# Optimization experiments

Measured on AMD Instinct MI355X. Metric: run time of the kernel, lower is better.

## Reference

```python
import jax, jax.numpy as jnp
import numpy as np

N, E, H, NIN, DD = 10000, 160000, 128, 128, 256
SCALE = 30.0
EPS = 1e-5

def _ln(x, g, b):
    mu = jnp.mean(x, axis=-1, keepdims=True)
    var = jnp.mean((x - mu) ** 2, axis=-1, keepdims=True)
    return (x - mu) * jax.lax.rsqrt(var + EPS) * g + b

def _gelu(x):
    return jax.nn.gelu(x, approximate=False)  # torch nn.GELU default (erf)

def setup_inputs() -> dict:
    key = jax.random.key(0)
    ks = jax.random.split(key, 16)
    def w(k, i, o):
        return jax.random.normal(k, (i, o), jnp.float32) * (1.0 / np.sqrt(i))
    return {
        "h_V": jax.random.normal(ks[0], (N, H), jnp.float32),
        "h_E": jax.random.normal(ks[1], (E, H + NIN), jnp.float32),
        "edge_idx": jax.random.randint(ks[2], (2, E), 0, N, jnp.int32),
        # message MLP: (H+NIN)->H, H->H
        "m_w0": w(ks[3], H + NIN, H), "m_b0": jnp.zeros((H,), jnp.float32),
        "m_w1": w(ks[4], H, H),       "m_b1": jnp.zeros((H,), jnp.float32),
        # dense MLP: H->DD, DD->DD, final DD->H
        "d_w0": w(ks[5], H, DD),  "d_b0": jnp.zeros((DD,), jnp.float32),
        "d_w1": w(ks[6], DD, DD), "d_b1": jnp.zeros((DD,), jnp.float32),
        "d_w2": w(ks[7], DD, H),  "d_b2": jnp.zeros((H,), jnp.float32),
        # LayerNorm params
        "g1": jnp.ones((H,), jnp.float32), "be1": jnp.zeros((H,), jnp.float32),
        "g2": jnp.ones((H,), jnp.float32), "be2": jnp.zeros((H,), jnp.float32),
    }

def reference(h_V, h_E, edge_idx, m_w0, m_b0, m_w1, m_b1,
              d_w0, d_b0, d_w1, d_b1, d_w2, d_b2, g1, be1, g2, be2):
    src_idx = edge_idx[0]
    # message MLP over edges (dropout = identity at inference)
    h = _gelu(h_E @ m_w0 + m_b0)
    h_message = _gelu(h @ m_w1 + m_b1)          # [E, H]
    # scatter-sum aggregate edges -> nodes
    dh = jax.ops.segment_sum(h_message, src_idx, num_segments=N) / SCALE
    h_V = _ln(h_V + dh, g1, be1)
    # dense MLP over nodes
    d = _gelu(h_V @ d_w0 + d_b0)
    d = _gelu(d @ d_w1 + d_b1)
    dh = d @ d_w2 + d_b2
    return _ln(h_V + dh, g2, be2)
```

## Files before the change

### kernel.cpp

```cpp
#include <hip/hip_runtime.h>
#include <hip/hip_bf16.h>


typedef __attribute__((ext_vector_type(8))) short bf16x8;
typedef __attribute__((ext_vector_type(4))) float f32x4;

__device__ __forceinline__ unsigned short f2bf(float f) {
  union { float f; unsigned u; } v; v.f = f;
  return (unsigned short)((v.u + 0x7fffu + ((v.u >> 16) & 1u)) >> 16);
}
__device__ __forceinline__ unsigned pk2bf(float a, float b) {
  __hip_bfloat162 h = __float22bfloat162_rn(make_float2(a, b));
  union { __hip_bfloat162 h; unsigned u; } v; v.h = h;
  return v.u;
}
__device__ __forceinline__ unsigned short bf1(float x) {
  return (unsigned short)pk2bf(x, x);
}
__device__ __forceinline__ float bf2f(unsigned s) {
  union { unsigned u; float f; } v; v.u = s << 16;
  return v.f;
}
__device__ __forceinline__ float gelu_f(float x) {
  float x2 = x * x;
  float u2 = x * fmaf(0.0713548162f, x2, 1.5957691216f);
  float e = __expf(u2);
  float r = __builtin_amdgcn_rcpf(e + 1.0f);
  float th = fmaf(-2.0f, r, 1.0f);
  float hx = 0.5f * x;
  return fmaf(hx, th, hx);
}

__global__ void k_pack(const float* __restrict__ mw0, const float* __restrict__ mw1,
                       const float* __restrict__ dw0, const float* __restrict__ dw1,
                       const float* __restrict__ dw2,
                       unsigned short* __restrict__ pw0, unsigned short* __restrict__ pw1,
                       unsigned short* __restrict__ pd0, unsigned short* __restrict__ pd1,
                       unsigned short* __restrict__ pd2,
                       int* __restrict__ counts, int Nn) {
  int g = blockIdx.x, lane = threadIdx.x;
  int z = g * 64 + lane;
  if (z < Nn) counts[z] = 0;
  const float* src; unsigned short* dst; int K, N, WC, base;
  if (g < 64)       { src = mw0; dst = pw0; K = 256; N = 128; WC = 128; base = 0; }
  else if (g < 96)  { src = mw1; dst = pw1; K = 128; N = 128; WC = 128; base = 64; }
  else if (g < 160) { src = dw0; dst = pd0; K = 128; N = 256; WC = 64; base = 96; }
  else if (g < 288) { src = dw1; dst = pd1; K = 256; N = 256; WC = 64; base = 160; }
  else              { src = dw2; dst = pd2; K = 256; N = 128; WC = 32; base = 288; }
  int lg = g - base;
  int KS = K >> 5, CTKS = (WC >> 4) * KS;
  int w = lg / CTKS, rem = lg % CTKS, ct = rem / KS, ks = rem % KS;
  int col = w * WC + ct * 16 + (lane & 15);
  int k0 = ks * 32 + (lane >> 4) * 8;
  unsigned short o[8];
#pragma unroll
  for (int j = 0; j < 8; ++j) o[j] = f2bf(src[(size_t)(k0 + j) * N + col]);
  uint4 u;
  u.x = (unsigned)o[0] | ((unsigned)o[1] << 16);
  u.y = (unsigned)o[2] | ((unsigned)o[3] << 16);
  u.z = (unsigned)o[4] | ((unsigned)o[5] << 16);
  u.w = (unsigned)o[6] | ((unsigned)o[7] << 16);
  *(uint4*)(dst + (size_t)(lg * 64 + lane) * 8) = u;
}

__global__ void k_hist(const int* __restrict__ eidx, int* __restrict__ counts, int E) {
  int e = blockIdx.x * 256 + threadIdx.x;
  if (e < E) atomicAdd(&counts[eidx[e]], 1);
}

__global__ __launch_bounds__(1024) void k_scan(const int* __restrict__ counts,
                                               int* __restrict__ row_start,
                                               int* __restrict__ cursor, int Nn) {
  __shared__ int sm[1024];
  int t = threadIdx.x;
  int chunk = (Nn + 1023) / 1024;
  int lo = t * chunk, hi = lo + chunk;
  if (hi > Nn) hi = Nn;
  int s = 0;
  for (int i = lo; i < hi; ++i) s += counts[i];
  sm[t] = s;
  __syncthreads();
  for (int o = 1; o < 1024; o <<= 1) {
    int u = (t >= o) ? sm[t - o] : 0;
    __syncthreads();
    sm[t] += u;
    __syncthreads();
  }
  int run = sm[t] - s;
  for (int i = lo; i < hi; ++i) {
    row_start[i] = run; cursor[i] = run; run += counts[i];
  }
  if (t == 1023) row_start[Nn] = sm[1023];
}

__global__ void k_scatter(const int* __restrict__ eidx, int* __restrict__ cursor,
                          int* __restrict__ eorder, int E) {
  int e = blockIdx.x * 256 + threadIdx.x;
  if (e < E) {
    int pos = atomicAdd(&cursor[eidx[e]], 1);
    eorder[pos] = e;
  }
}

__global__ __launch_bounds__(512, 2) void k_edge(
    const float* __restrict__ hE, const unsigned short* __restrict__ pw0,
    const unsigned short* __restrict__ pw1, const float* __restrict__ b0,
    const float* __restrict__ b1, unsigned short* __restrict__ hmsg, int E) {
  __shared__ __align__(16) char lds[131072];
  const int tid = threadIdx.x;
  const int wid = tid >> 6, lane = tid & 63;
  const int l15 = lane & 15, lhi = lane >> 4;
  char* Hw = lds + 98304 + wid * 4096;

  {
    const uint4* s0 = (const uint4*)pw0;
    const uint4* s1 = (const uint4*)pw1;
    uint4* d = (uint4*)lds;
#pragma unroll
    for (int i = 0; i < 12; ++i) {
      int idx = i * 512 + tid;
      d[idx] = (idx < 4096) ? s0[idx] : s1[idx - 4096];
    }
  }
  float bb0[8], bb1[8];
#pragma unroll
  for (int ct = 0; ct < 8; ++ct) {
    bb0[ct] = b0[ct * 16 + l15];
    bb1[ct] = b1[ct * 16 + l15];
  }
  __syncthreads();

  const int TILES = (E + 15) >> 4;
  const int WSLOTS = gridDim.x * 8;
  int t = blockIdx.x * 8 + wid;
  if (t >= TILES) return;

  f32x4 av[16];
  {
    int rowA = t * 16 + l15; rowA = rowA < E ? rowA : E - 1;
    const float* ap = hE + (size_t)rowA * 256 + lhi * 8;
#pragma unroll
    for (int ks = 0; ks < 8; ++ks) {
      av[2 * ks]     = *(const f32x4*)(ap + ks * 32);
      av[2 * ks + 1] = *(const f32x4*)(ap + ks * 32 + 4);
    }
  }

  for (; t < TILES; t += WSLOTS) {
    const int tn = t + WSLOTS;
    bf16x8 af[8];
#pragma unroll
    for (int ks = 0; ks < 8; ++ks) {
      union { unsigned u[4]; bf16x8 v; } pk;
      pk.u[0] = pk2bf(av[2 * ks][0], av[2 * ks][1]);
      pk.u[1] = pk2bf(av[2 * ks][2], av[2 * ks][3]);
      pk.u[2] = pk2bf(av[2 * ks + 1][0], av[2 * ks + 1][1]);
      pk.u[3] = pk2bf(av[2 * ks + 1][2], av[2 * ks + 1][3]);
      af[ks] = pk.v;
    }
    if (tn < TILES) {
      int rowA = tn * 16 + l15; rowA = rowA < E ? rowA : E - 1;
      const float* ap = hE + (size_t)rowA * 256 + lhi * 8;
#pragma unroll
      for (int ks = 0; ks < 8; ++ks) {
        av[2 * ks]     = *(const f32x4*)(ap + ks * 32);
        av[2 * ks + 1] = *(const f32x4*)(ap + ks * 32 + 4);
      }
    }

    f32x4 acc[8];
#pragma unroll
    for (int ct = 0; ct < 8; ++ct) {
      float b = bb0[ct];
      acc[ct][0] = b; acc[ct][1] = b; acc[ct][2] = b; acc[ct][3] = b;
    }
#pragma unroll
    for (int ks = 0; ks < 8; ++ks)
#pragma unroll
      for (int ct = 0; ct < 8; ++ct) {
        bf16x8 b = *(bf16x8*)(lds + (ct * 8 + ks) * 1024 + lane * 16);
        acc[ct] = __builtin_amdgcn_mfma_f32_16x16x32_bf16(af[ks], b, acc[ct], 0, 0, 0);
      }
#pragma unroll
    for (int ct = 0; ct < 8; ++ct)
#pragma unroll
      for (int j = 0; j < 4; ++j) {
        int r = lhi * 4 + j, col = ct * 16 + l15;
        *(unsigned short*)(Hw + r * 256 + ((col * 2) ^ ((r & 7) << 4))) =
            bf1(gelu_f(acc[ct][j]));
      }

    f32x4 acc2[8];
#pragma unroll
    for (int ct = 0; ct < 8; ++ct) {
      float b = bb1[ct];
      acc2[ct][0] = b; acc2[ct][1] = b; acc2[ct][2] = b; acc2[ct][3] = b;
    }
#pragma unroll
    for (int ks = 0; ks < 4; ++ks) {
      bf16x8 a = *(bf16x8*)(Hw + l15 * 256 + ((ks * 64 + lhi * 16) ^ ((l15 & 7) << 4)));
#pragma unroll
      for (int ct = 0; ct < 8; ++ct) {
        bf16x8 b = *(bf16x8*)(lds + 65536 + (ct * 4 + ks) * 1024 + lane * 16);
        acc2[ct] = __builtin_amdgcn_mfma_f32_16x16x32_bf16(a, b, acc2[ct], 0, 0, 0);
      }
    }
    const int row0 = t * 16;
#pragma unroll
    for (int ct = 0; ct < 8; ++ct)
#pragma unroll
      for (int j = 0; j < 4; ++j) {
        int r = row0 + lhi * 4 + j;
        if (r < E) {
          int col = ct * 16 + l15;
          hmsg[(size_t)r * 128 + col] = bf1(gelu_f(acc2[ct][j]));
        }
      }
  }
}

__global__ __launch_bounds__(256) void k_aggln(
    const unsigned* __restrict__ hmsg, const float2* __restrict__ hV,
    const int* __restrict__ row_start, const int* __restrict__ eorder,
    const float* __restrict__ g1, const float* __restrict__ be1,
    float2* __restrict__ hv1f, unsigned* __restrict__ hv1b, int Nn) {
  int wid = threadIdx.x >> 6, lane = threadIdx.x & 63;
  int node = blockIdx.x * 4 + wid;
  if (node >= Nn) return;
  int s = row_start[node], e = row_start[node + 1];
  float s0 = 0.f, s1 = 0.f;
  int i = s;
  for (; i + 3 < e; i += 4) {
    int e0 = eorder[i], e1 = eorder[i + 1], e2 = eorder[i + 2], e3 = eorder[i + 3];
    unsigned v0 = hmsg[(size_t)e0 * 64 + lane];
    unsigned v1 = hmsg[(size_t)e1 * 64 + lane];
    unsigned v2 = hmsg[(size_t)e2 * 64 + lane];
    unsigned v3 = hmsg[(size_t)e3 * 64 + lane];
    s0 += bf2f(v0 & 0xffffu) + bf2f(v1 & 0xffffu) + bf2f(v2 & 0xffffu) + bf2f(v3 & 0xffffu);
    s1 += bf2f(v0 >> 16) + bf2f(v1 >> 16) + bf2f(v2 >> 16) + bf2f(v3 >> 16);
  }
  for (; i < e; ++i) {
    unsigned v = hmsg[(size_t)eorder[i] * 64 + lane];
    s0 += bf2f(v & 0xffffu);
    s1 += bf2f(v >> 16);
  }
  float2 hv = hV[(size_t)node * 64 + lane];
  float x0 = hv.x + s0 * (1.f / 30.f);
  float x1 = hv.y + s1 * (1.f / 30.f);
  float sum = x0 + x1, sq = x0 * x0 + x1 * x1;
#pragma unroll
  for (int off = 32; off > 0; off >>= 1) {
    sum += __shfl_xor(sum, off);
    sq += __shfl_xor(sq, off);
  }
  float mu = sum * (1.f / 128.f);
  float var = sq * (1.f / 128.f) - mu * mu;
  float rs = rsqrtf(var + 1e-5f);
  int c = lane * 2;
  float y0 = (x0 - mu) * rs * g1[c] + be1[c];
  float y1 = (x1 - mu) * rs * g1[c + 1] + be1[c + 1];
  hv1f[(size_t)node * 64 + lane] = make_float2(y0, y1);
  hv1b[(size_t)node * 64 + lane] = (unsigned)pk2bf(y0, y1);
}

__global__ __launch_bounds__(256, 4) void k_node(
    const unsigned short* __restrict__ xb, const unsigned short* __restrict__ pd0,
    const unsigned short* __restrict__ pd1, const unsigned short* __restrict__ pd2,
    const float* __restrict__ db0, const float* __restrict__ db1,
    const float* __restrict__ db2, const float* __restrict__ hv1f,
    const float* __restrict__ g2, const float* __restrict__ be2,
    float* __restrict__ out, int Nn) {
  __shared__ __align__(16) char lds[8192 + 16384 + 16384];
  char* A0 = lds;
  char* D0 = lds + 8192;
  char* D1 = lds + 8192 + 16384;
  float* Y = (float*)D0;
  const int tid = threadIdx.x, wid = tid >> 6, lane = tid & 63;
  const int l15 = lane & 15, lhi = lane >> 4;
  const int row0 = blockIdx.x * 32;

  {
    int idx = tid;
    int r = idx >> 3, c = idx & 7;
    uint4 v = make_uint4(0u, 0u, 0u, 0u);
    if (row0 + r < Nn) v = ((const uint4*)xb)[(size_t)(row0 + r) * 16 + c * 2];
    *(uint4*)(A0 + r * 256 + ((c * 32) ^ ((r & 7) << 4))) = v;
    uint4 v2 = make_uint4(0u, 0u, 0u, 0u);
    if (row0 + r < Nn) v2 = ((const uint4*)xb)[(size_t)(row0 + r) * 16 + c * 2 + 1];
    *(uint4*)(A0 + r * 256 + (((c * 32) + 16) ^ ((r & 7) << 4))) = v2;
  }
  __syncthreads();

  {
    f32x4 acc[2][4];
#pragma unroll
    for (int ct = 0; ct < 4; ++ct) {
      float b = db0[wid * 64 + ct * 16 + l15];
#pragma unroll
      for (int mt = 0; mt < 2; ++mt) {
        acc[mt][ct][0] = b; acc[mt][ct][1] = b; acc[mt][ct][2] = b; acc[mt][ct][3] = b;
      }
    }
#pragma unroll
    for (int ks = 0; ks < 4; ++ks) {
      bf16x8 a[2];
#pragma unroll
      for (int mt = 0; mt < 2; ++mt) {
        int row = mt * 16 + l15;
        a[mt] = *(bf16x8*)(A0 + row * 256 + ((ks * 64 + lhi * 16) ^ ((row & 7) << 4)));
      }
#pragma unroll
      for (int ct = 0; ct < 4; ++ct) {
        uint4 bv = ((const uint4*)pd0)[(size_t)(wid * 16 + ct * 4 + ks) * 64 + lane];
        bf16x8 b = *(bf16x8*)&bv;
#pragma unroll
        for (int mt = 0; mt < 2; ++mt)
          acc[mt][ct] = __builtin_amdgcn_mfma_f32_16x16x32_bf16(a[mt], b, acc[mt][ct], 0, 0, 0);
      }
    }
#pragma unroll
    for (int ct = 0; ct < 4; ++ct) {
      int col = wid * 64 + ct * 16 + l15;
#pragma unroll
      for (int mt = 0; mt < 2; ++mt)
#pragma unroll
        for (int j = 0; j < 4; ++j) {
          int r = mt * 16 + lhi * 4 + j;
          *(unsigned short*)(D0 + r * 512 + ((col * 2) ^ ((r & 7) << 4))) =
              bf1(gelu_f(acc[mt][ct][j]));
        }
    }
  }
  __syncthreads();

  {
    f32x4 acc[2][4];
#pragma unroll
    for (int ct = 0; ct < 4; ++ct) {
      float b = db1[wid * 64 + ct * 16 + l15];
#pragma unroll
      for (int mt = 0; mt < 2; ++mt) {
        acc[mt][ct][0] = b; acc[mt][ct][1] = b; acc[mt][ct][2] = b; acc[mt][ct][3] = b;
      }
    }
#pragma unroll
    for (int ks = 0; ks < 8; ++ks) {
      bf16x8 a[2];
#pragma unroll
      for (int mt = 0; mt < 2; ++mt) {
        int row = mt * 16 + l15;
        a[mt] = *(bf16x8*)(D0 + row * 512 + ((ks * 64 + lhi * 16) ^ ((row & 7) << 4)));
      }
#pragma unroll
      for (int ct = 0; ct < 4; ++ct) {
        uint4 bv = ((const uint4*)pd1)[(size_t)(wid * 32 + ct * 8 + ks) * 64 + lane];
        bf16x8 b = *(bf16x8*)&bv;
#pragma unroll
        for (int mt = 0; mt < 2; ++mt)
          acc[mt][ct] = __builtin_amdgcn_mfma_f32_16x16x32_bf16(a[mt], b, acc[mt][ct], 0, 0, 0);
      }
    }
#pragma unroll
    for (int ct = 0; ct < 4; ++ct) {
      int col = wid * 64 + ct * 16 + l15;
#pragma unroll
      for (int mt = 0; mt < 2; ++mt)
#pragma unroll
        for (int j = 0; j < 4; ++j) {
          int r = mt * 16 + lhi * 4 + j;
          *(unsigned short*)(D1 + r * 512 + ((col * 2) ^ ((r & 7) << 4))) =
              bf1(gelu_f(acc[mt][ct][j]));
        }
    }
  }
  __syncthreads();

  {
    f32x4 acc[2][2];
#pragma unroll
    for (int ct = 0; ct < 2; ++ct) {
      float b = db2[wid * 32 + ct * 16 + l15];
#pragma unroll
      for (int mt = 0; mt < 2; ++mt) {
        acc[mt][ct][0] = b; acc[mt][ct][1] = b; acc[mt][ct][2] = b; acc[mt][ct][3] = b;
      }
    }
#pragma unroll
    for (int ks = 0; ks < 8; ++ks) {
      bf16x8 a[2];
#pragma unroll
      for (int mt = 0; mt < 2; ++mt) {
        int row = mt * 16 + l15;
        a[mt] = *(bf16x8*)(D1 + row * 512 + ((ks * 64 + lhi * 16) ^ ((row & 7) << 4)));
      }
#pragma unroll
      for (int ct = 0; ct < 2; ++ct) {
        uint4 bv = ((const uint4*)pd2)[(size_t)(wid * 16 + ct * 8 + ks) * 64 + lane];
        bf16x8 b = *(bf16x8*)&bv;
#pragma unroll
        for (int mt = 0; mt < 2; ++mt)
          acc[mt][ct] = __builtin_amdgcn_mfma_f32_16x16x32_bf16(a[mt], b, acc[mt][ct], 0, 0, 0);
      }
    }
    __syncthreads();
#pragma unroll
    for (int ct = 0; ct < 2; ++ct) {
      int col = wid * 32 + ct * 16 + l15;
#pragma unroll
      for (int mt = 0; mt < 2; ++mt)
#pragma unroll
        for (int j = 0; j < 4; ++j) {
          int r = mt * 16 + lhi * 4 + j;
          int grow = row0 + r;
          float res = (grow < Nn) ? hv1f[(size_t)grow * 128 + col] : 0.f;
          Y[r * 128 + col] = acc[mt][ct][j] + res;
        }
    }
  }
  __syncthreads();

  float g2a = g2[lane * 2], g2b = g2[lane * 2 + 1];
  float ba = be2[lane * 2], bbx = be2[lane * 2 + 1];
  for (int ii = 0; ii < 8; ++ii) {
    int r = wid * 8 + ii;
    int grow = row0 + r;
    if (grow >= Nn) continue;
    float2 xy = *(float2*)&Y[r * 128 + lane * 2];
    float sum = xy.x + xy.y, sq = xy.x * xy.x + xy.y * xy.y;
#pragma unroll
    for (int off = 32; off > 0; off >>= 1) {
      sum += __shfl_xor(sum, off);
      sq += __shfl_xor(sq, off);
    }
    float mu = sum * (1.f / 128.f);
    float var = sq * (1.f / 128.f) - mu * mu;
    float rs = rsqrtf(var + 1e-5f);
    float y0 = (xy.x - mu) * rs * g2a + ba;
    float y1 = (xy.y - mu) * rs * g2b + bbx;
    *(float2*)&out[(size_t)grow * 128 + lane * 2] = make_float2(y0, y1);
  }
}

extern "C" void kernel_launch(void* const* d_in, const int* in_sizes, int n_in,
                              void* d_out, int out_size, void* d_ws, size_t ws_size,
                              hipStream_t stream) {
  const float* hV  = (const float*)d_in[0];
  const float* hE  = (const float*)d_in[1];
  const int* eidx  = (const int*)d_in[2];
  const float* mw0 = (const float*)d_in[3];
  const float* mb0 = (const float*)d_in[4];
  const float* mw1 = (const float*)d_in[5];
  const float* mb1 = (const float*)d_in[6];
  const float* dw0 = (const float*)d_in[7];
  const float* db0 = (const float*)d_in[8];
  const float* dw1 = (const float*)d_in[9];
  const float* db1 = (const float*)d_in[10];
  const float* dw2 = (const float*)d_in[11];
  const float* db2 = (const float*)d_in[12];
  const float* g1  = (const float*)d_in[13];
  const float* be1 = (const float*)d_in[14];
  const float* g2  = (const float*)d_in[15];
  const float* be2 = (const float*)d_in[16];
  const int Nn = in_sizes[0] / 128;
  const int E  = in_sizes[1] / 256;

  char* ws = (char*)d_ws;
  size_t off = 0;
  auto alloc = [&](size_t bytes) -> char* {
    off = (off + 255) & ~(size_t)255;
    char* p = ws + off;
    off += bytes;
    return p;
  };
  unsigned short* hmsg = (unsigned short*)alloc((size_t)E * 128 * 2);
  float* hv1f          = (float*)alloc((size_t)Nn * 128 * 4);
  unsigned short* hv1b = (unsigned short*)alloc((size_t)Nn * 128 * 2);
  unsigned short* pw0  = (unsigned short*)alloc(32768 * 2);
  unsigned short* pw1  = (unsigned short*)alloc(16384 * 2);
  unsigned short* pd0  = (unsigned short*)alloc(32768 * 2);
  unsigned short* pd1  = (unsigned short*)alloc(65536 * 2);
  unsigned short* pd2  = (unsigned short*)alloc(32768 * 2);
  int* counts    = (int*)alloc((size_t)Nn * 4);
  int* row_start = (int*)alloc((size_t)(Nn + 1) * 4);
  int* cursor    = (int*)alloc((size_t)Nn * 4);
  int* eorder    = (int*)alloc((size_t)E * 4);

  k_pack<<<352, 64, 0, stream>>>(mw0, mw1, dw0, dw1, dw2, pw0, pw1, pd0, pd1, pd2,
                                 counts, Nn);
  k_hist<<<(E + 255) / 256, 256, 0, stream>>>(eidx, counts, E);
  k_scan<<<1, 1024, 0, stream>>>(counts, row_start, cursor, Nn);
  k_scatter<<<(E + 255) / 256, 256, 0, stream>>>(eidx, cursor, eorder, E);
  k_edge<<<256, 512, 0, stream>>>(hE, pw0, pw1, mb0, mb1, hmsg, E);
  k_aggln<<<(Nn + 3) / 4, 256, 0, stream>>>((const unsigned*)hmsg, (const float2*)hV,
                                            row_start, eorder, g1, be1,
                                            (float2*)hv1f, (unsigned*)hv1b, Nn);
  const int nt = (Nn + 31) / 32;
  k_node<<<nt, 256, 0, stream>>>(hv1b, pd0, pd1, pd2, db0, db1, db2,
                                 hv1f, g2, be2, (float*)d_out, Nn);
}
```

Before: 135.1 us.

## Process two 16-row edge tiles per wave to reuse LDS weight fragments

The edge message MLP kernel now has each wave handle 32 edge rows per iteration instead of 16. Each weight fragment loaded from LDS feeds two MFMAs, which halves LDS traffic per matrix instruction, and the per-wave scratch buffer is doubled to hold both tiles' intermediate activations. In exchange, the cross-iteration software prefetch of the next tile's h_E rows is dropped, LDS use grows to 160KB, and register pressure rises under the existing launch bounds, with a risk of spills.

```diff
diff --git a/kernel.cpp b/kernel.cpp
--- a/kernel.cpp
+++ b/kernel.cpp
@@ -106,11 +106,11 @@
     const float* __restrict__ hE, const unsigned short* __restrict__ pw0,
     const unsigned short* __restrict__ pw1, const float* __restrict__ b0,
     const float* __restrict__ b1, unsigned short* __restrict__ hmsg, int E) {
-  __shared__ __align__(16) char lds[131072];
+  __shared__ __align__(16) char lds[163840];
   const int tid = threadIdx.x;
   const int wid = tid >> 6, lane = tid & 63;
   const int l15 = lane & 15, lhi = lane >> 4;
-  char* Hw = lds + 98304 + wid * 4096;
+  char* Hw = lds + 98304 + wid * 8192;
 
   {
     const uint4* s0 = (const uint4*)pw0;
@@ -130,91 +130,104 @@
   }
   __syncthreads();
 
-  const int TILES = (E + 15) >> 4;
+  const int TILES = (E + 31) >> 5;
   const int WSLOTS = gridDim.x * 8;
-  int t = blockIdx.x * 8 + wid;
-  if (t >= TILES) return;
-
-  f32x4 av[16];
-  {
-    int rowA = t * 16 + l15; rowA = rowA < E ? rowA : E - 1;
-    const float* ap = hE + (size_t)rowA * 256 + lhi * 8;
-#pragma unroll
-    for (int ks = 0; ks < 8; ++ks) {
-      av[2 * ks]     = *(const f32x4*)(ap + ks * 32);
-      av[2 * ks + 1] = *(const f32x4*)(ap + ks * 32 + 4);
-    }
-  }
-
-  for (; t < TILES; t += WSLOTS) {
-    const int tn = t + WSLOTS;
-    bf16x8 af[8];
-#pragma unroll
-    for (int ks = 0; ks < 8; ++ks) {
-      union { unsigned u[4]; bf16x8 v; } pk;
-      pk.u[0] = pk2bf(av[2 * ks][0], av[2 * ks][1]);
-      pk.u[1] = pk2bf(av[2 * ks][2], av[2 * ks][3]);
-      pk.u[2] = pk2bf(av[2 * ks + 1][0], av[2 * ks + 1][1]);
-      pk.u[3] = pk2bf(av[2 * ks + 1][2], av[2 * ks + 1][3]);
-      af[ks] = pk.v;
-    }
-    if (tn < TILES) {
-      int rowA = tn * 16 + l15; rowA = rowA < E ? rowA : E - 1;
-      const float* ap = hE + (size_t)rowA * 256 + lhi * 8;
+  for (int t = blockIdx.x * 8 + wid; t < TILES; t += WSLOTS) {
+    const int row0 = t * 32;
+    int r0 = row0 + l15;      r0 = r0 < E ? r0 : E - 1;
+    int r1 = row0 + 16 + l15; r1 = r1 < E ? r1 : E - 1;
+    const float* ap0 = hE + (size_t)r0 * 256 + lhi * 8;
+    const float* ap1 = hE + (size_t)r1 * 256 + lhi * 8;
+
+    bf16x8 af0[8], af1[8];
+    {
+      f32x4 av0[16], av1[16];
 #pragma unroll
       for (int ks = 0; ks < 8; ++ks) {
-        av[2 * ks]     = *(const f32x4*)(ap + ks * 32);
-        av[2 * ks + 1] = *(const f32x4*)(ap + ks * 32 + 4);
-      }
-    }
-
-    f32x4 acc[8];
+        av0[2 * ks]     = *(const f32x4*)(ap0 + ks * 32);
+        av0[2 * ks + 1] = *(const f32x4*)(ap0 + ks * 32 + 4);
+      }
+#pragma unroll
+      for (int ks = 0; ks < 8; ++ks) {
+        av1[2 * ks]     = *(const f32x4*)(ap1 + ks * 32);
+        av1[2 * ks + 1] = *(const f32x4*)(ap1 + ks * 32 + 4);
+      }
+#pragma unroll
+      for (int ks = 0; ks < 8; ++ks) {
+        union { unsigned u[4]; bf16x8 v; } p0, p1;
+        p0.u[0] = pk2bf(av0[2 * ks][0], av0[2 * ks][1]);
+        p0.u[1] = pk2bf(av0[2 * ks][2], av0[2 * ks][3]);
+        p0.u[2] = pk2bf(av0[2 * ks + 1][0], av0[2 * ks + 1][1]);
+        p0.u[3] = pk2bf(av0[2 * ks + 1][2], av0[2 * ks + 1][3]);
+        af0[ks] = p0.v;
+        p1.u[0] = pk2bf(av1[2 * ks][0], av1[2 * ks][1]);
+        p1.u[1] = pk2bf(av1[2 * ks][2], av1[2 * ks][3]);
+        p1.u[2] = pk2bf(av1[2 * ks + 1][0], av1[2 * ks + 1][1]);
+        p1.u[3] = pk2bf(av1[2 * ks + 1][2], av1[2 * ks + 1][3]);
+        af1[ks] = p1.v;
+      }
+    }
+
+    f32x4 acc0[8], acc1[8];
 #pragma unroll
     for (int ct = 0; ct < 8; ++ct) {
       float b = bb0[ct];
-      acc[ct][0] = b; acc[ct][1] = b; acc[ct][2] = b; acc[ct][3] = b;
-    }
-#pragma unroll
-    for (int ks = 0; ks < 8; ++ks)
+      acc0[ct][0] = b; acc0[ct][1] = b; acc0[ct][2] = b; acc0[ct][3] = b;
+      acc1[ct] = acc0[ct];
+    }
+#pragma unroll
+    for (int ks = 0; ks < 8; ++ks) {
+      bf16x8 bfr[8];
+#pragma unroll
+      for (int ct = 0; ct < 8; ++ct)
+        bfr[ct] = *(bf16x8*)(lds + (ct * 8 + ks) * 1024 + lane * 16);
 #pragma unroll
       for (int ct = 0; ct < 8; ++ct) {
-        bf16x8 b = *(bf16x8*)(lds + (ct * 8 + ks) * 1024 + lane * 16);
-        acc[ct] = __builtin_amdgcn_mfma_f32_16x16x32_bf16(af[ks], b, acc[ct], 0, 0, 0);
-      }
+        acc0[ct] = __builtin_amdgcn_mfma_f32_16x16x32_bf16(af0[ks], bfr[ct], acc0[ct], 0, 0, 0);
+        acc1[ct] = __builtin_amdgcn_mfma_f32_16x16x32_bf16(af1[ks], bfr[ct], acc1[ct], 0, 0, 0);
+      }
+    }
 #pragma unroll
     for (int ct = 0; ct < 8; ++ct)
 #pragma unroll
       for (int j = 0; j < 4; ++j) {
-        int r = lhi * 4 + j, col = ct * 16 + l15;
-        *(unsigned short*)(Hw + r * 256 + ((col * 2) ^ ((r & 7) << 4))) =
-            bf1(gelu_f(acc[ct][j]));
-      }
-
-    f32x4 acc2[8];
+        int rr = lhi * 4 + j, col = ct * 16 + l15;
+        int sw = (col * 2) ^ ((rr & 7) << 4);
+        *(unsigned short*)(Hw + rr * 256 + sw) = bf1(gelu_f(acc0[ct][j]));
+        *(unsigned short*)(Hw + (16 + rr) * 256 + sw) = bf1(gelu_f(acc1[ct][j]));
+      }
+
+    f32x4 acc20[8], acc21[8];
 #pragma unroll
     for (int ct = 0; ct < 8; ++ct) {
       float b = bb1[ct];
-      acc2[ct][0] = b; acc2[ct][1] = b; acc2[ct][2] = b; acc2[ct][3] = b;
+      acc20[ct][0] = b; acc20[ct][1] = b; acc20[ct][2] = b; acc20[ct][3] = b;
+      acc21[ct] = acc20[ct];
     }
 #pragma unroll
     for (int ks = 0; ks < 4; ++ks) {
-      bf16x8 a = *(bf16x8*)(Hw + l15 * 256 + ((ks * 64 + lhi * 16) ^ ((l15 & 7) << 4)));
+      int off = (ks * 64 + lhi * 16) ^ ((l15 & 7) << 4);
+      bf16x8 a0 = *(bf16x8*)(Hw + l15 * 256 + off);
+      bf16x8 a1 = *(bf16x8*)(Hw + (16 + l15) * 256 + off);
+      bf16x8 bfr[8];
+#pragma unroll
+      for (int ct = 0; ct < 8; ++ct)
+        bfr[ct] = *(bf16x8*)(lds + 65536 + (ct * 4 + ks) * 1024 + lane * 16);
 #pragma unroll
       for (int ct = 0; ct < 8; ++ct) {
-        bf16x8 b = *(bf16x8*)(lds + 65536 + (ct * 4 + ks) * 1024 + lane * 16);
-        acc2[ct] = __builtin_amdgcn_mfma_f32_16x16x32_bf16(a, b, acc2[ct], 0, 0, 0);
-      }
-    }
-    const int row0 = t * 16;
+        acc20[ct] = __builtin_amdgcn_mfma_f32_16x16x32_bf16(a0, bfr[ct], acc20[ct], 0, 0, 0);
+        acc21[ct] = __builtin_amdgcn_mfma_f32_16x16x32_bf16(a1, bfr[ct], acc21[ct], 0, 0, 0);
+      }
+    }
 #pragma unroll
     for (int ct = 0; ct < 8; ++ct)
 #pragma unroll
       for (int j = 0; j < 4; ++j) {
-        int r = row0 + lhi * 4 + j;
-        if (r < E) {
-          int col = ct * 16 + l15;
-          hmsg[(size_t)r * 128 + col] = bf1(gelu_f(acc2[ct][j]));
-        }
+        int col = ct * 16 + l15;
+        int ra = row0 + lhi * 4 + j;
+        if (ra < E) hmsg[(size_t)ra * 128 + col] = bf1(gelu_f(acc20[ct][j]));
+        int rb = ra + 16;
+        if (rb < E) hmsg[(size_t)rb * 128 + col] = bf1(gelu_f(acc21[ct][j]));
       }
   }
 }
```

Result: slower. 139.1 us (+3.0%).
